# Performance work log

Measured on AMD Instinct MI355X. Metric: run time of the kernel, lower is better.

Reference implementation:

```python
import jax, jax.numpy as jnp
import numpy as np

EMB = 512
GP = 128
NH = 8
HD = EMB // NH  # 64
B = 2
S = 1024


def _rel_shift(x):
    # Faithful port of DoubleAttentionLayer._rel_shift (pads dim 1, reinterprets
    # (B, J+1, K, n) as (J+1, B, K, n), drops first slice). Row-major reshape
    # semantics match torch .view on contiguous tensors exactly.
    Bsz, J, K, N = x.shape
    zp = jnp.zeros((Bsz, 1, K, N), x.dtype)
    xp = jnp.concatenate([zp, x], axis=1).reshape(J + 1, Bsz, K, N)
    return xp[1:].reshape(Bsz, J, K, N)


def _layernorm(x):
    # nn.LayerNorm(emb_dim, elementwise_affine=False), eps=1e-5
    m = jnp.mean(x, axis=-1, keepdims=True)
    v = jnp.var(x, axis=-1, keepdims=True)
    return (x - m) / jnp.sqrt(v + 1e-5)


def _attention(q, k, v, Bc, Bp, gpe, mask, Wp_w, Wp_b):
    Bsz, J, E = q.shape
    K = k.shape[1]
    # content scores
    qc = jnp.tanh((q + Bc).reshape(Bsz, J, NH, HD))
    kh = jnp.tanh(k.reshape(Bsz, K, NH, HD))
    ctx = jnp.einsum('bjnd,bknd->bjkn', qc, kh)
    # position scores (tanh before reshape in source for qp -- elementwise, same math)
    qp = jnp.tanh(q + Bp).reshape(Bsz, J, NH, HD)
    kp = jnp.tanh((gpe @ Wp_w + Wp_b).reshape(Bsz, -1, NH, HD))
    pos = jnp.einsum('bjnd,bknd->bjkn', qp, kp)
    pad = ctx.shape[2] - pos.shape[2]  # static; 0 in this configuration
    if pad > 0:
        # replicate-pad pos at front of k dim; constant(0)-pad mask (torch F.pad defaults)
        pos = jnp.concatenate([jnp.broadcast_to(pos[:, :, :1], (Bsz, J, pad, NH)), pos], axis=2)
        mask = jnp.concatenate([jnp.zeros(mask.shape[:2] + (pad, mask.shape[3]), mask.dtype), mask], axis=2)
    pos = _rel_shift(pos)
    att = (ctx + pos) / (HD ** 0.5) - 1e30 * mask
    att = jax.nn.softmax(att, axis=2)
    vh = jnp.tanh(v.reshape(Bsz, K, NH, HD))
    return jnp.einsum('bjkn,bknd->bjnd', att, vh).reshape(Bsz, J, E)


def setup_inputs() -> dict:
    key = jax.random.key(0)
    ks = jax.random.split(key, 12)
    u_emb = jax.random.normal(ks[0], (B, S, EMB), jnp.float32)
    f_emb = jax.random.normal(ks[1], (B, S, EMB), jnp.float32)
    gpe = jax.random.normal(ks[2], (B, S, GP), jnp.float32)
    # causal masks: 1 where attention is disallowed, broadcast over heads
    causal = (1.0 - jnp.tril(jnp.ones((S, S), jnp.float32)))[None, :, :, None]
    u_mask = jnp.broadcast_to(causal, (B, S, S, 1))
    f_mask = jnp.broadcast_to(causal, (B, S, S, 1))
    w = 0.02
    Wq_w = w * jax.random.normal(ks[3], (EMB, EMB), jnp.float32)
    Wq_b = jnp.zeros((EMB,), jnp.float32)
    Wkv_w = w * jax.random.normal(ks[4], (EMB, 2 * EMB), jnp.float32)
    Wkv_b = jnp.zeros((2 * EMB,), jnp.float32)
    Wp_w = w * jax.random.normal(ks[5], (GP, EMB), jnp.float32)
    Wp_b = jnp.zeros((EMB,), jnp.float32)
    Wu_w = w * jax.random.normal(ks[6], (EMB, EMB), jnp.float32)
    Wu_b = jnp.zeros((EMB,), jnp.float32)
    Bfc = 0.2 * jax.random.normal(ks[7], (1, 1, EMB), jnp.float32)
    Bfp = 0.2 * jax.random.normal(ks[8], (1, 1, EMB), jnp.float32)
    Buc = 0.2 * jax.random.normal(ks[9], (1, 1, EMB), jnp.float32)
    Bup = 0.2 * jax.random.normal(ks[10], (1, 1, EMB), jnp.float32)
    return {"u_emb": u_emb, "f_emb": f_emb, "gpe": gpe, "u_mask": u_mask, "f_mask": f_mask,
            "Wq_w": Wq_w, "Wq_b": Wq_b, "Wkv_w": Wkv_w, "Wkv_b": Wkv_b,
            "Wp_w": Wp_w, "Wp_b": Wp_b, "Wu_w": Wu_w, "Wu_b": Wu_b,
            "Bfc": Bfc, "Bfp": Bfp, "Buc": Buc, "Bup": Bup}


def reference(u_emb, f_emb, gpe, u_mask, f_mask, Wq_w, Wq_b, Wkv_w, Wkv_b,
              Wp_w, Wp_b, Wu_w, Wu_b, Bfc, Bfp, Buc, Bup):
    # first_part=True path: f_mem = f_emb (memory buffer registration has no output effect)
    q_u = f_emb @ Wu_w + Wu_b
    kv = f_emb @ Wkv_w + Wkv_b
    k, v = jnp.split(kv, 2, axis=-1)
    u_out = _layernorm(u_emb + _attention(q_u, k, v, Buc, Bup, gpe, u_mask, Wp_w, Wp_b))
    # last_layer=False: second attention over f stream
    q_f = f_emb @ Wq_w + Wq_b
    f_out = _layernorm(f_emb + _attention(q_f, k, v, Bfc, Bfp, gpe, f_mask, Wp_w, Wp_b))
    return (u_out, f_out)
```

## Files before the change

### kernel.cpp

```cpp
#include <hip/hip_runtime.h>
#include <math.h>

#define EMB 512
#define NH 8
#define HD 64
#define BB 2
#define SS 1024
#define ROWS (BB * SS)

typedef __attribute__((ext_vector_type(8))) short bhalf8;
typedef __attribute__((ext_vector_type(4))) float f32x4;
typedef __attribute__((ext_vector_type(8))) unsigned short us8;
typedef unsigned short ushort_t;

__device__ __forceinline__ unsigned short f2bf(float x) {
  unsigned u = __float_as_uint(x);
  u = (u + 0x7FFFu + ((u >> 16) & 1u)) >> 16;
  return (unsigned short)u;
}
__device__ __forceinline__ float bf2f(unsigned short v) {
  return __uint_as_float(((unsigned)v) << 16);
}
__device__ __forceinline__ float fast_tanh(float x) {
  x = fminf(15.f, fmaxf(-15.f, x));
  const float e = __expf(2.f * x);
  return (e - 1.f) / (e + 1.f);
}

__global__ __launch_bounds__(256, 3) void projpe_kernel(
    const float* __restrict__ f_emb, const float* __restrict__ gpe,
    const float* __restrict__ Wu, const float* __restrict__ Wq,
    const float* __restrict__ Wkv, const float* __restrict__ Wp,
    const float* __restrict__ Wu_b, const float* __restrict__ Wq_b,
    const float* __restrict__ Wkv_b, const float* __restrict__ Wp_b,
    const float* __restrict__ Buc, const float* __restrict__ Bup,
    const float* __restrict__ Bfc, const float* __restrict__ Bfp,
    ushort_t* __restrict__ Qcomb, ushort_t* __restrict__ Kcomb,
    ushort_t* __restrict__ vhT) {
  const int bx = blockIdx.x;
  const int mb = blockIdx.y * 128;
  const int tid = threadIdx.x;
  const int w = tid >> 6, lane = tid & 63;
  const int ln = lane & 15, quad = lane >> 4;
  const int wm = (w >> 1) * 64, wn = (w & 1) * 32;

  __shared__ __align__(16) ushort_t sA[128 * 72];
  __shared__ __align__(16) ushort_t sB[64 * 72];

  if (bx == 0 && blockIdx.y == 0) {
    const int t2 = tid >> 7, rem = tid & 127;
    const int h = rem >> 4, d4 = (rem & 15) * 4;
    *(ushort4*)&Qcomb[((size_t)t2 * ROWS + 1023) * 1024 + h * 128 + 64 + d4] =
        make_ushort4(0, 0, 0, 0);
  }

  const bool isPe = (bx >= 32);
  const int nb = isPe ? 0 : bx * 64;
  const int npbase = isPe ? (bx - 32) * 64 : 0;
  const float* Af = isPe ? gpe : f_emb;
  const int lda = isPe ? 128 : 512;
  const int trips = isPe ? 2 : 8;

  const float* Wsrc;
  int Nw, coff;
  if (isPe) { Wsrc = Wp; Nw = 512; coff = npbase; }
  else if (nb < 512) { Wsrc = Wu; Nw = 512; coff = nb; }
  else if (nb < 1024) { Wsrc = Wq; Nw = 512; coff = nb - 512; }
  else { Wsrc = Wkv; Nw = 1024; coff = nb - 1024; }

  const int bn = tid & 63;
  const int bk0 = (tid >> 6) * 16;

  f32x4 acc[4][2];
#pragma unroll
  for (int rt = 0; rt < 4; ++rt)
#pragma unroll
    for (int ct = 0; ct < 2; ++ct) acc[rt][ct] = (f32x4){0.f, 0.f, 0.f, 0.f};

  float4 qa[8];
  float qbw[16];
#pragma unroll
  for (int i = 0; i < 4; ++i) {
    const int idx = tid + i * 256;
    const size_t base = (size_t)(mb + (idx >> 3)) * lda + (idx & 7) * 8;
    qa[2 * i] = *(const float4*)&Af[base];
    qa[2 * i + 1] = *(const float4*)&Af[base + 4];
  }
#pragma unroll
  for (int j = 0; j < 16; ++j)
    qbw[j] = Wsrc[(size_t)(bk0 + j) * Nw + coff + bn];

  for (int t0 = 0; t0 < trips; ++t0) {
    __syncthreads();
#pragma unroll
    for (int i = 0; i < 4; ++i) {
      const int idx = tid + i * 256;
      us8 o;
      const float4 a = qa[2 * i], b = qa[2 * i + 1];
      o[0] = f2bf(a.x); o[1] = f2bf(a.y); o[2] = f2bf(a.z); o[3] = f2bf(a.w);
      o[4] = f2bf(b.x); o[5] = f2bf(b.y); o[6] = f2bf(b.z); o[7] = f2bf(b.w);
      *(us8*)&sA[(idx >> 3) * 72 + (idx & 7) * 8] = o;
    }
    {
      us8 o0, o1;
#pragma unroll
      for (int j = 0; j < 8; ++j) {
        o0[j] = f2bf(qbw[j]);
        o1[j] = f2bf(qbw[8 + j]);
      }
      *(us8*)&sB[bn * 72 + bk0] = o0;
      *(us8*)&sB[bn * 72 + bk0 + 8] = o1;
    }
    __syncthreads();
    if (t0 < trips - 1) {
      const int k1 = (t0 + 1) * 64;
#pragma unroll
      for (int i = 0; i < 4; ++i) {
        const int idx = tid + i * 256;
        const size_t base = (size_t)(mb + (idx >> 3)) * lda + k1 + (idx & 7) * 8;
        qa[2 * i] = *(const float4*)&Af[base];
        qa[2 * i + 1] = *(const float4*)&Af[base + 4];
      }
#pragma unroll
      for (int j = 0; j < 16; ++j)
        qbw[j] = Wsrc[(size_t)(k1 + bk0 + j) * Nw + coff + bn];
    }
#pragma unroll
    for (int kc = 0; kc < 2; ++kc) {
      bhalf8 af[4], bf_[2];
#pragma unroll
      for (int rt = 0; rt < 4; ++rt)
        af[rt] =
            *(const bhalf8*)&sA[(wm + rt * 16 + ln) * 72 + kc * 32 + quad * 8];
#pragma unroll
      for (int ct = 0; ct < 2; ++ct)
        bf_[ct] =
            *(const bhalf8*)&sB[(wn + ct * 16 + ln) * 72 + kc * 32 + quad * 8];
#pragma unroll
      for (int rt = 0; rt < 4; ++rt)
#pragma unroll
        for (int ct = 0; ct < 2; ++ct)
          acc[rt][ct] = __builtin_amdgcn_mfma_f32_16x16x32_bf16(
              af[rt], bf_[ct], acc[rt][ct], 0, 0, 0);
    }
  }

  __syncthreads();
  ushort_t* sOut = sA;

  if (!isPe && nb >= 1536) {
#pragma unroll
    for (int ct = 0; ct < 2; ++ct) {
      const int nl = wn + ct * 16 + ln;
      const float wb = Wkv_b[nb + nl - 1024];
#pragma unroll
      for (int rt = 0; rt < 4; ++rt)
#pragma unroll
        for (int r = 0; r < 4; ++r) {
          const int ml = wm + rt * 16 + quad * 4 + r;
          sOut[nl * 136 + ml] = f2bf(fast_tanh(acc[rt][ct][r] + wb));
        }
    }
    __syncthreads();
    const int b = mb >> 10, mo = mb & 1023;
#pragma unroll
    for (int i = 0; i < 4; ++i) {
      const int idx = tid + i * 256;
      const int nl = idx >> 4, m8 = (idx & 15) * 8;
      const us8 v = *(const us8*)&sOut[nl * 136 + m8];
      *(us8*)&vhT[((size_t)b * 512 + (nb - 1536) + nl) * 1024 + mo + m8] = v;
    }
  } else {
    const float* WB =
        isPe ? Wp_b : (nb < 512 ? Wu_b : (nb < 1024 ? Wq_b : Wkv_b));
    const int woff =
        isPe ? npbase : (nb < 512 ? nb : (nb < 1024 ? nb - 512 : nb - 1024));
    const bool rawDump = (!isPe && nb < 1024);
#pragma unroll
    for (int ct = 0; ct < 2; ++ct) {
      const int nl = wn + ct * 16 + ln;
      const float wb = WB[woff + nl];
#pragma unroll
      for (int rt = 0; rt < 4; ++rt)
#pragma unroll
        for (int r = 0; r < 4; ++r) {
          const int ml = wm + rt * 16 + quad * 4 + r;
          const float v = acc[rt][ct][r] + wb;
          sOut[ml * 72 + nl] = f2bf(rawDump ? v : fast_tanh(v));
        }
    }
    __syncthreads();
#pragma unroll
    for (int i = 0; i < 4; ++i) {
      const int idx = tid + i * 256;
      const int rr = idx >> 3, c8 = (idx & 7) * 8;
      const int m = mb + rr;
      const us8 v = *(const us8*)&sOut[rr * 72 + c8];
      if (isPe) {
        const int n = npbase + c8;
        const int h = n >> 6;
        *(us8*)&Kcomb[(size_t)m * 1024 + h * 128 + 64 + (n & 63)] = v;
      } else if (nb < 1024) {
        const int strm = nb >= 512 ? 1 : 0;
        const int n = (nb - strm * 512) + c8;
        const int h = n >> 6;
        const float* BC = strm ? Bfc : Buc;
        const float* BP = strm ? Bfp : Bup;
        float bcA[8], bpA[8];
        *(float4*)&bcA[0] = *(const float4*)&BC[n];
        *(float4*)&bcA[4] = *(const float4*)&BC[n + 4];
        *(float4*)&bpA[0] = *(const float4*)&BP[n];
        *(float4*)&bpA[4] = *(const float4*)&BP[n + 4];
        us8 oc, op;
#pragma unroll
        for (int jj = 0; jj < 8; ++jj) {
          const float vv = bf2f((unsigned short)v[jj]);
          oc[jj] = f2bf(fast_tanh(vv + bcA[jj]));
          op[jj] = f2bf(fast_tanh(vv + bpA[jj]));
        }
        *(us8*)&Qcomb[((size_t)strm * ROWS + m) * 1024 + h * 128 + (n & 63)] =
            oc;
        if (m != 0) {
          const int mp = (m < 1024) ? m - 1 : m;
          *(us8*)&Qcomb[((size_t)strm * ROWS + mp) * 1024 + h * 128 + 64 +
                        (n & 63)] = op;
        }
      } else {
        const int n = (nb - 1024) + c8;
        const int h = n >> 6;
        *(us8*)&Kcomb[(size_t)m * 1024 + h * 128 + (n & 63)] = v;
      }
    }
  }
}

__global__ __launch_bounds__(256, 2) void attn_kernel(
    const ushort_t* __restrict__ Qcomb, const ushort_t* __restrict__ Kcomb,
    const ushort_t* __restrict__ vhT, ushort_t* __restrict__ attO) {
  const int bid = blockIdx.x;
  const int tid = threadIdx.x;
  const int w = tid >> 6, lane = tid & 63;
  const int ln = lane & 15, quad = lane >> 4;

  __shared__ __align__(16) ushort_t sQ[64 * 136];
  __shared__ __align__(16) ushort_t sK[64 * 136];
  __shared__ __align__(16) ushort_t sV[64 * 72];
  __shared__ __align__(16) ushort_t sP[64 * 72];

  const int jt = (bid < 256) ? (15 - (bid >> 5)) : ((bid - 256) >> 5);
  const int c = bid & 31, t = c >> 4, b = (c >> 3) & 1, h = c & 7;

  uint4 qq[4], pk[4], pv[2];
#pragma unroll
  for (int i = 0; i < 4; ++i) {
    const int idx = tid + i * 256;
    qq[i] = *(const uint4*)&Qcomb[((size_t)t * ROWS + b * SS + jt * 64 +
                                   (idx >> 4)) * 1024 + h * 128 +
                                  (idx & 15) * 8];
    pk[i] = *(const uint4*)&Kcomb[((size_t)b * SS + (idx >> 4)) * 1024 +
                                  h * 128 + (idx & 15) * 8];
  }
#pragma unroll
  for (int i = 0; i < 2; ++i) {
    const int idx = tid + i * 256;
    pv[i] = *(const uint4*)&vhT[((size_t)b * 512 + h * 64 + (idx >> 3)) * 1024 +
                                (idx & 7) * 8];
  }
#pragma unroll
  for (int i = 0; i < 4; ++i) {
    const int idx = tid + i * 256;
    *(uint4*)&sQ[(idx >> 4) * 136 + (idx & 15) * 8] = qq[i];
  }
  __syncthreads();

  bhalf8 aq[4];
#pragma unroll
  for (int kc = 0; kc < 4; ++kc)
    aq[kc] = *(const bhalf8*)&sQ[(w * 16 + ln) * 136 + kc * 32 + quad * 8];

  f32x4 oacc[4];
#pragma unroll
  for (int ct = 0; ct < 4; ++ct) oacc[ct] = (f32x4){0.f, 0.f, 0.f, 0.f};
  float lsum[4] = {0.f, 0.f, 0.f, 0.f};

  for (int kt = 0; kt <= jt; ++kt) {
    if (kt > 0) __syncthreads();
#pragma unroll
    for (int i = 0; i < 4; ++i) {
      const int idx = tid + i * 256;
      *(uint4*)&sK[(idx >> 4) * 136 + (idx & 15) * 8] = pk[i];
    }
#pragma unroll
    for (int i = 0; i < 2; ++i) {
      const int idx = tid + i * 256;
      *(uint4*)&sV[(idx >> 3) * 72 + (idx & 7) * 8] = pv[i];
    }
    __syncthreads();
    if (kt < jt) {
      const int k1 = (kt + 1) * 64;
#pragma unroll
      for (int i = 0; i < 4; ++i) {
        const int idx = tid + i * 256;
        pk[i] = *(const uint4*)&Kcomb[((size_t)b * SS + k1 + (idx >> 4)) *
                                          1024 + h * 128 + (idx & 15) * 8];
      }
#pragma unroll
      for (int i = 0; i < 2; ++i) {
        const int idx = tid + i * 256;
        pv[i] = *(const uint4*)&vhT[((size_t)b * 512 + h * 64 + (idx >> 3)) *
                                        1024 + k1 + (idx & 7) * 8];
      }
    }

    f32x4 sacc[4];
#pragma unroll
    for (int ct = 0; ct < 4; ++ct) {
      sacc[ct] = (f32x4){0.f, 0.f, 0.f, 0.f};
#pragma unroll
      for (int kc = 0; kc < 4; ++kc) {
        const bhalf8 bk =
            *(const bhalf8*)&sK[(ct * 16 + ln) * 136 + kc * 32 + quad * 8];
        sacc[ct] = __builtin_amdgcn_mfma_f32_16x16x32_bf16(aq[kc], bk,
                                                           sacc[ct], 0, 0, 0);
      }
    }

    const bool diag = (kt == jt);
#pragma unroll
    for (int ct = 0; ct < 4; ++ct)
#pragma unroll
      for (int r = 0; r < 4; ++r) {
        float p;
        if (diag && (ct * 16 + ln > w * 16 + quad * 4 + r))
          p = 0.f;
        else
          p = __expf(sacc[ct][r] * 0.125f - 16.f);
        sacc[ct][r] = p;
        lsum[r] += p;
      }

#pragma unroll
    for (int ct = 0; ct < 4; ++ct)
#pragma unroll
      for (int r = 0; r < 4; ++r)
        sP[(w * 16 + quad * 4 + r) * 72 + ct * 16 + ln] = f2bf(sacc[ct][r]);

#pragma unroll
    for (int kc = 0; kc < 2; ++kc) {
      const bhalf8 ap =
          *(const bhalf8*)&sP[(w * 16 + ln) * 72 + kc * 32 + quad * 8];
#pragma unroll
      for (int ct = 0; ct < 4; ++ct) {
        const bhalf8 bv =
            *(const bhalf8*)&sV[(ct * 16 + ln) * 72 + kc * 32 + quad * 8];
        oacc[ct] = __builtin_amdgcn_mfma_f32_16x16x32_bf16(ap, bv, oacc[ct],
                                                           0, 0, 0);
      }
    }
  }

#pragma unroll
  for (int r = 0; r < 4; ++r) {
    float s = lsum[r];
    s += __shfl_xor(s, 1);
    s += __shfl_xor(s, 2);
    s += __shfl_xor(s, 4);
    s += __shfl_xor(s, 8);
    const float inv = 1.f / s;
    const int j = jt * 64 + w * 16 + quad * 4 + r;
    const size_t orow = ((size_t)t * ROWS + b * SS + j) * 512 + h * 64;
#pragma unroll
    for (int ct = 0; ct < 4; ++ct)
      attO[orow + ct * 16 + ln] = f2bf(oacc[ct][r] * inv);
  }
}

__global__ __launch_bounds__(64) void ln_kernel(
    const float* __restrict__ u_emb, const float* __restrict__ f_emb,
    const ushort_t* __restrict__ attO, float* __restrict__ out) {
  const int rid = blockIdx.x;
  const int t = rid >> 11, row = rid & 2047;
  const float* resid = t ? f_emb : u_emb;
  const int tid = threadIdx.x;
  const size_t base = (size_t)row * 512;
  const size_t obase = ((size_t)t * ROWS + row) * 512;
  const int o = tid * 8;

  const us8 a = *(const us8*)&attO[obase + o];
  const float4 r0 = *(const float4*)&resid[base + o];
  const float4 r1 = *(const float4*)&resid[base + o + 4];
  float y[8];
  y[0] = r0.x + bf2f((unsigned short)a[0]);
  y[1] = r0.y + bf2f((unsigned short)a[1]);
  y[2] = r0.z + bf2f((unsigned short)a[2]);
  y[3] = r0.w + bf2f((unsigned short)a[3]);
  y[4] = r1.x + bf2f((unsigned short)a[4]);
  y[5] = r1.y + bf2f((unsigned short)a[5]);
  y[6] = r1.z + bf2f((unsigned short)a[6]);
  y[7] = r1.w + bf2f((unsigned short)a[7]);

  float s = 0.f, q = 0.f;
#pragma unroll
  for (int i = 0; i < 8; ++i) {
    s += y[i];
    q += y[i] * y[i];
  }
#pragma unroll
  for (int off = 1; off < 64; off <<= 1) {
    s += __shfl_xor(s, off);
    q += __shfl_xor(q, off);
  }
  const float mean = s * (1.f / 512.f);
  const float var = q * (1.f / 512.f) - mean * mean;
  const float rstd = rsqrtf(var + 1e-5f);

  float4 o0, o1;
  o0.x = (y[0] - mean) * rstd; o0.y = (y[1] - mean) * rstd;
  o0.z = (y[2] - mean) * rstd; o0.w = (y[3] - mean) * rstd;
  o1.x = (y[4] - mean) * rstd; o1.y = (y[5] - mean) * rstd;
  o1.z = (y[6] - mean) * rstd; o1.w = (y[7] - mean) * rstd;
  *(float4*)&out[obase + o] = o0;
  *(float4*)&out[obase + o + 4] = o1;
}

extern "C" void kernel_launch(void* const* d_in, const int* in_sizes, int n_in,
                              void* d_out, int out_size, void* d_ws,
                              size_t ws_size, hipStream_t stream) {
  (void)in_sizes; (void)n_in; (void)out_size; (void)ws_size;
  const float* u_emb = (const float*)d_in[0];
  const float* f_emb = (const float*)d_in[1];
  const float* gpe = (const float*)d_in[2];
  const float* Wq_w = (const float*)d_in[5];
  const float* Wq_b = (const float*)d_in[6];
  const float* Wkv_w = (const float*)d_in[7];
  const float* Wkv_b = (const float*)d_in[8];
  const float* Wp_w = (const float*)d_in[9];
  const float* Wp_b = (const float*)d_in[10];
  const float* Wu_w = (const float*)d_in[11];
  const float* Wu_b = (const float*)d_in[12];
  const float* Bfc = (const float*)d_in[13];
  const float* Bfp = (const float*)d_in[14];
  const float* Buc = (const float*)d_in[15];
  const float* Bup = (const float*)d_in[16];
  float* out = (float*)d_out;

  ushort_t* ws = (ushort_t*)d_ws;
  const size_t SZ = (size_t)ROWS * EMB;
  ushort_t* Qcomb = ws;
  ushort_t* Kcomb = ws + 4 * SZ;
  ushort_t* vhT = ws + 6 * SZ;
  ushort_t* attO = ws + 7 * SZ;

  dim3 blk(256);
  hipLaunchKernelGGL(projpe_kernel, dim3(40, 16), blk, 0, stream, f_emb, gpe,
                     Wu_w, Wq_w, Wkv_w, Wp_w, Wu_b, Wq_b, Wkv_b, Wp_b, Buc,
                     Bup, Bfc, Bfp, Qcomb, Kcomb, vhT);
  hipLaunchKernelGGL(attn_kernel, dim3(512), blk, 0, stream, Qcomb, Kcomb, vhT,
                     attO);
  hipLaunchKernelGGL(ln_kernel, dim3(4096), dim3(64), 0, stream, u_emb, f_emb,
                     attO, out);
}
```

Before: 170.8 us.

## Split long causal attention rows across two blocks and merge partials in layernorm

Query tiles in the upper half (jt 8-15) now have their key range split between two blocks. Each block writes an unnormalized partial output and a row sum, and the layernorm kernel adds the two partials and normalizes. Without a running max, the fixed exp offset makes the two partials combine exactly. The change also loads Q fragments straight from global memory instead of staging them in shared memory, raises occupancy to 3 blocks per SM, replaces the rounded bf16 conversion of P with truncation, and packs 4 rows per layernorm block. The aim is better load balance and more blocks in flight, at the cost of extra partial-buffer traffic and a small precision loss.

```diff
diff --git a/kernel.cpp b/kernel.cpp
--- a/kernel.cpp
+++ b/kernel.cpp
@@ -234,57 +234,70 @@
   }
 }
 
-__global__ __launch_bounds__(256, 2) void attn_kernel(
+__global__ __launch_bounds__(256, 3) void attn_kernel(
     const ushort_t* __restrict__ Qcomb, const ushort_t* __restrict__ Kcomb,
-    const ushort_t* __restrict__ vhT, ushort_t* __restrict__ attO) {
+    const ushort_t* __restrict__ vhT, ushort_t* __restrict__ attO,
+    ushort_t* __restrict__ Opart, float* __restrict__ lpart) {
   const int bid = blockIdx.x;
   const int tid = threadIdx.x;
   const int w = tid >> 6, lane = tid & 63;
   const int ln = lane & 15, quad = lane >> 4;
 
-  __shared__ __align__(16) ushort_t sQ[64 * 136];
   __shared__ __align__(16) ushort_t sK[64 * 136];
   __shared__ __align__(16) ushort_t sV[64 * 72];
   __shared__ __align__(16) ushort_t sP[64 * 72];
 
-  const int jt = (bid < 256) ? (15 - (bid >> 5)) : ((bid - 256) >> 5);
-  const int c = bid & 31, t = c >> 4, b = (c >> 3) & 1, h = c & 7;
-
-  uint4 qq[4], pk[4], pv[2];
+  int jt, kt0, kt1, half;
+  bool isHalf;
+  const int c = bid & 31;
+  if (bid < 512) {
+    isHalf = true;
+    const int uu = bid >> 5;
+    jt = 15 - (uu >> 1);
+    half = uu & 1;
+    const int h1 = (jt + 2) >> 1;
+    kt0 = half ? h1 : 0;
+    kt1 = half ? jt : (h1 - 1);
+  } else {
+    isHalf = false;
+    half = 0;
+    jt = 7 - ((bid - 512) >> 5);
+    kt0 = 0;
+    kt1 = jt;
+  }
+  const int t = c >> 4, b = (c >> 3) & 1, h = c & 7;
+
+  bhalf8 aq[4];
+  {
+    const size_t qbase =
+        ((size_t)t * ROWS + b * SS + jt * 64 + w * 16 + ln) * 1024 + h * 128 +
+        quad * 8;
+#pragma unroll
+    for (int kc = 0; kc < 4; ++kc)
+      aq[kc] = *(const bhalf8*)&Qcomb[qbase + kc * 32];
+  }
+
+  uint4 pk[4], pv[2];
 #pragma unroll
   for (int i = 0; i < 4; ++i) {
     const int idx = tid + i * 256;
-    qq[i] = *(const uint4*)&Qcomb[((size_t)t * ROWS + b * SS + jt * 64 +
-                                   (idx >> 4)) * 1024 + h * 128 +
-                                  (idx & 15) * 8];
-    pk[i] = *(const uint4*)&Kcomb[((size_t)b * SS + (idx >> 4)) * 1024 +
-                                  h * 128 + (idx & 15) * 8];
+    pk[i] = *(const uint4*)&Kcomb[((size_t)b * SS + kt0 * 64 + (idx >> 4)) *
+                                      1024 + h * 128 + (idx & 15) * 8];
   }
 #pragma unroll
   for (int i = 0; i < 2; ++i) {
     const int idx = tid + i * 256;
     pv[i] = *(const uint4*)&vhT[((size_t)b * 512 + h * 64 + (idx >> 3)) * 1024 +
-                                (idx & 7) * 8];
-  }
-#pragma unroll
-  for (int i = 0; i < 4; ++i) {
-    const int idx = tid + i * 256;
-    *(uint4*)&sQ[(idx >> 4) * 136 + (idx & 15) * 8] = qq[i];
-  }
-  __syncthreads();
-
-  bhalf8 aq[4];
-#pragma unroll
-  for (int kc = 0; kc < 4; ++kc)
-    aq[kc] = *(const bhalf8*)&sQ[(w * 16 + ln) * 136 + kc * 32 + quad * 8];
+                                kt0 * 64 + (idx & 7) * 8];
+  }
 
   f32x4 oacc[4];
 #pragma unroll
   for (int ct = 0; ct < 4; ++ct) oacc[ct] = (f32x4){0.f, 0.f, 0.f, 0.f};
   float lsum[4] = {0.f, 0.f, 0.f, 0.f};
 
-  for (int kt = 0; kt <= jt; ++kt) {
-    if (kt > 0) __syncthreads();
+  for (int kt = kt0; kt <= kt1; ++kt) {
+    if (kt > kt0) __syncthreads();
 #pragma unroll
     for (int i = 0; i < 4; ++i) {
       const int idx = tid + i * 256;
@@ -296,7 +309,7 @@
       *(uint4*)&sV[(idx >> 3) * 72 + (idx & 7) * 8] = pv[i];
     }
     __syncthreads();
-    if (kt < jt) {
+    if (kt < kt1) {
       const int k1 = (kt + 1) * 64;
 #pragma unroll
       for (int i = 0; i < 4; ++i) {
@@ -343,7 +356,8 @@
     for (int ct = 0; ct < 4; ++ct)
 #pragma unroll
       for (int r = 0; r < 4; ++r)
-        sP[(w * 16 + quad * 4 + r) * 72 + ct * 16 + ln] = f2bf(sacc[ct][r]);
+        sP[(w * 16 + quad * 4 + r) * 72 + ct * 16 + ln] =
+            (ushort_t)(__float_as_uint(sacc[ct][r]) >> 16);
 
 #pragma unroll
     for (int kc = 0; kc < 2; ++kc) {
@@ -366,38 +380,60 @@
     s += __shfl_xor(s, 2);
     s += __shfl_xor(s, 4);
     s += __shfl_xor(s, 8);
-    const float inv = 1.f / s;
     const int j = jt * 64 + w * 16 + quad * 4 + r;
-    const size_t orow = ((size_t)t * ROWS + b * SS + j) * 512 + h * 64;
-#pragma unroll
-    for (int ct = 0; ct < 4; ++ct)
-      attO[orow + ct * 16 + ln] = f2bf(oacc[ct][r] * inv);
-  }
-}
-
-__global__ __launch_bounds__(64) void ln_kernel(
+    if (!isHalf) {
+      const float inv = 1.f / s;
+      const size_t orow = ((size_t)t * ROWS + b * SS + j) * 512 + h * 64;
+#pragma unroll
+      for (int ct = 0; ct < 4; ++ct)
+        attO[orow + ct * 16 + ln] = f2bf(oacc[ct][r] * inv);
+    } else {
+      const int slot = half * 4 + t * 2 + b;
+      const size_t prow = ((size_t)slot * 512 + (j - 512)) * 512 + h * 64;
+#pragma unroll
+      for (int ct = 0; ct < 4; ++ct)
+        Opart[prow + ct * 16 + ln] = f2bf(oacc[ct][r]);
+      if (ln == 0)
+        lpart[((size_t)slot * 512 + (j - 512)) * 8 + h] = s;
+    }
+  }
+}
+
+__global__ __launch_bounds__(256) void ln_kernel(
     const float* __restrict__ u_emb, const float* __restrict__ f_emb,
-    const ushort_t* __restrict__ attO, float* __restrict__ out) {
-  const int rid = blockIdx.x;
+    const ushort_t* __restrict__ attO, const ushort_t* __restrict__ Opart,
+    const float* __restrict__ lpart, float* __restrict__ out) {
+  const int rid = blockIdx.x * 4 + (threadIdx.x >> 6);
+  const int lane = threadIdx.x & 63;
   const int t = rid >> 11, row = rid & 2047;
+  const int b = row >> 10, j = row & 1023;
   const float* resid = t ? f_emb : u_emb;
-  const int tid = threadIdx.x;
   const size_t base = (size_t)row * 512;
   const size_t obase = ((size_t)t * ROWS + row) * 512;
-  const int o = tid * 8;
-
-  const us8 a = *(const us8*)&attO[obase + o];
+  const int o = lane * 8;
+
   const float4 r0 = *(const float4*)&resid[base + o];
   const float4 r1 = *(const float4*)&resid[base + o + 4];
+  float ra[8] = {r0.x, r0.y, r0.z, r0.w, r1.x, r1.y, r1.z, r1.w};
   float y[8];
-  y[0] = r0.x + bf2f((unsigned short)a[0]);
-  y[1] = r0.y + bf2f((unsigned short)a[1]);
-  y[2] = r0.z + bf2f((unsigned short)a[2]);
-  y[3] = r0.w + bf2f((unsigned short)a[3]);
-  y[4] = r1.x + bf2f((unsigned short)a[4]);
-  y[5] = r1.y + bf2f((unsigned short)a[5]);
-  y[6] = r1.z + bf2f((unsigned short)a[6]);
-  y[7] = r1.w + bf2f((unsigned short)a[7]);
+  if (j < 512) {
+    const us8 a = *(const us8*)&attO[obase + o];
+#pragma unroll
+    for (int i = 0; i < 8; ++i) y[i] = ra[i] + bf2f((unsigned short)a[i]);
+  } else {
+    const int h = lane >> 3;
+    const int s0 = t * 2 + b, s1 = 4 + t * 2 + b;
+    const size_t pr = (size_t)(j - 512);
+    const float l = lpart[((size_t)s0 * 512 + pr) * 8 + h] +
+                    lpart[((size_t)s1 * 512 + pr) * 8 + h];
+    const float inv = 1.f / l;
+    const us8 a0 = *(const us8*)&Opart[((size_t)s0 * 512 + pr) * 512 + o];
+    const us8 a1 = *(const us8*)&Opart[((size_t)s1 * 512 + pr) * 512 + o];
+#pragma unroll
+    for (int i = 0; i < 8; ++i)
+      y[i] = ra[i] + (bf2f((unsigned short)a0[i]) +
+                      bf2f((unsigned short)a1[i])) * inv;
+  }
 
   float s = 0.f, q = 0.f;
 #pragma unroll
@@ -450,13 +486,15 @@
   ushort_t* Kcomb = ws + 4 * SZ;
   ushort_t* vhT = ws + 6 * SZ;
   ushort_t* attO = ws + 7 * SZ;
+  ushort_t* Opart = ws + 9 * SZ;
+  float* lpart = (float*)(ws + 11 * SZ);
 
   dim3 blk(256);
   hipLaunchKernelGGL(projpe_kernel, dim3(40, 16), blk, 0, stream, f_emb, gpe,
                      Wu_w, Wq_w, Wkv_w, Wp_w, Wu_b, Wq_b, Wkv_b, Wp_b, Buc,
                      Bup, Bfc, Bfp, Qcomb, Kcomb, vhT);
-  hipLaunchKernelGGL(attn_kernel, dim3(512), blk, 0, stream, Qcomb, Kcomb, vhT,
-                     attO);
-  hipLaunchKernelGGL(ln_kernel, dim3(4096), dim3(64), 0, stream, u_emb, f_emb,
-                     attO, out);
-}
+  hipLaunchKernelGGL(attn_kernel, dim3(768), blk, 0, stream, Qcomb, Kcomb, vhT,
+                     attO, Opart, lpart);
+  hipLaunchKernelGGL(ln_kernel, dim3(1024), blk, 0, stream, u_emb, f_emb, attO,
+                     Opart, lpart, out);
+}
```

After: 170.9 us. About the same (+0.1%).

## Balance causal attention with stream-K tile split, atomics, and async LDS loads

Applied to the files above, without the earlier changes.

Replaces the per-row-tile attention blocks with a stream-K style schedule. The 4352 causal (jt,kt) tiles are spread evenly over 512 blocks, 8 or 9 tiles each, and partial numerators and row sums are accumulated with fp32 atomics into buffers zeroed by the projection kernel. K and V are staged through double-buffered LDS via global_load_lds with an XOR swizzle, and Q is loaded straight into registers. The goal is to remove the load imbalance of the triangular workload and hide load latency. In exchange it adds atomic traffic, a larger fp32 workspace, a truncating bf16 conversion for P, and a final normalisation step in the layernorm kernel, which is also regrouped to four rows per 256-thread block.

```diff
diff --git a/kernel.cpp b/kernel.cpp
--- a/kernel.cpp
+++ b/kernel.cpp
@@ -13,6 +13,13 @@
 typedef __attribute__((ext_vector_type(8))) unsigned short us8;
 typedef unsigned short ushort_t;
 
+typedef const __attribute__((address_space(1))) void gas_void;
+typedef __attribute__((address_space(3))) void las_void;
+
+__device__ __forceinline__ void gl2lds16(const void* g, void* l) {
+  __builtin_amdgcn_global_load_lds((gas_void*)g, (las_void*)l, 16, 0, 0);
+}
+
 __device__ __forceinline__ unsigned short f2bf(float x) {
   unsigned u = __float_as_uint(x);
   u = (u + 0x7FFFu + ((u >> 16) & 1u)) >> 16;
@@ -27,7 +34,7 @@
   return (e - 1.f) / (e + 1.f);
 }
 
-__global__ __launch_bounds__(256, 3) void projpe_kernel(
+__global__ __launch_bounds__(256, 4) void projpe_kernel(
     const float* __restrict__ f_emb, const float* __restrict__ gpe,
     const float* __restrict__ Wu, const float* __restrict__ Wq,
     const float* __restrict__ Wkv, const float* __restrict__ Wp,
@@ -36,7 +43,8 @@
     const float* __restrict__ Buc, const float* __restrict__ Bup,
     const float* __restrict__ Bfc, const float* __restrict__ Bfp,
     ushort_t* __restrict__ Qcomb, ushort_t* __restrict__ Kcomb,
-    ushort_t* __restrict__ vhT) {
+    ushort_t* __restrict__ vhT, float* __restrict__ Onum,
+    float* __restrict__ lpart) {
   const int bx = blockIdx.x;
   const int mb = blockIdx.y * 128;
   const int tid = threadIdx.x;
@@ -47,7 +55,16 @@
   __shared__ __align__(16) ushort_t sA[128 * 72];
   __shared__ __align__(16) ushort_t sB[64 * 72];
 
-  if (bx == 0 && blockIdx.y == 0) {
+  const int fb = blockIdx.y * 40 + bx;
+  if (fb < 512) {
+    const float4 z4 = {0.f, 0.f, 0.f, 0.f};
+#pragma unroll
+    for (int i = 0; i < 4; ++i)
+      ((float4*)Onum)[(size_t)fb * 1024 + i * 256 + tid] = z4;
+  } else {
+    lpart[(fb - 512) * 256 + tid] = 0.f;
+  }
+  if (fb == 0) {
     const int t2 = tid >> 7, rem = tid & 127;
     const int h = rem >> 4, d4 = (rem & 15) * 4;
     *(ushort4*)&Qcomb[((size_t)t2 * ROWS + 1023) * 1024 + h * 128 + 64 + d4] =
@@ -236,80 +253,82 @@
 
 __global__ __launch_bounds__(256, 2) void attn_kernel(
     const ushort_t* __restrict__ Qcomb, const ushort_t* __restrict__ Kcomb,
-    const ushort_t* __restrict__ vhT, ushort_t* __restrict__ attO) {
+    const ushort_t* __restrict__ vhT, float* __restrict__ Onum,
+    float* __restrict__ lpart) {
   const int bid = blockIdx.x;
   const int tid = threadIdx.x;
   const int w = tid >> 6, lane = tid & 63;
   const int ln = lane & 15, quad = lane >> 4;
 
-  __shared__ __align__(16) ushort_t sQ[64 * 136];
-  __shared__ __align__(16) ushort_t sK[64 * 136];
-  __shared__ __align__(16) ushort_t sV[64 * 72];
+  __shared__ __align__(16) ushort_t sK[2 * 64 * 128];
+  __shared__ __align__(16) ushort_t sV[2 * 64 * 64];
   __shared__ __align__(16) ushort_t sP[64 * 72];
 
-  const int jt = (bid < 256) ? (15 - (bid >> 5)) : ((bid - 256) >> 5);
-  const int c = bid & 31, t = c >> 4, b = (c >> 3) & 1, h = c & 7;
-
-  uint4 qq[4], pk[4], pv[2];
-#pragma unroll
-  for (int i = 0; i < 4; ++i) {
-    const int idx = tid + i * 256;
-    qq[i] = *(const uint4*)&Qcomb[((size_t)t * ROWS + b * SS + jt * 64 +
-                                   (idx >> 4)) * 1024 + h * 128 +
-                                  (idx & 15) * 8];
-    pk[i] = *(const uint4*)&Kcomb[((size_t)b * SS + (idx >> 4)) * 1024 +
-                                  h * 128 + (idx & 15) * 8];
-  }
-#pragma unroll
-  for (int i = 0; i < 2; ++i) {
-    const int idx = tid + i * 256;
-    pv[i] = *(const uint4*)&vhT[((size_t)b * 512 + h * 64 + (idx >> 3)) * 1024 +
-                                (idx & 7) * 8];
-  }
-#pragma unroll
-  for (int i = 0; i < 4; ++i) {
-    const int idx = tid + i * 256;
-    *(uint4*)&sQ[(idx >> 4) * 136 + (idx & 15) * 8] = qq[i];
-  }
-  __syncthreads();
+  const int G0 = (bid * 17) >> 1;
+  const int G1 = ((bid + 1) * 17) >> 1;
+  const int cnt = G1 - G0;
+
+  int c = G0 / 136;
+  int u = G0 - c * 136;
+  int jt = (int)((sqrtf(8.f * u + 1.f) - 1.f) * 0.5f);
+  while ((jt + 1) * (jt + 2) / 2 <= u) ++jt;
+  while (jt * (jt + 1) / 2 > u) --jt;
+  int kt = u - jt * (jt + 1) / 2;
+  int t = c >> 4, b = (c >> 3) & 1, h = c & 7;
+
+  const int l4 = lane >> 4, p15 = lane & 15;
+  const int l3 = lane >> 3, l7 = lane & 7;
+#define STAGE_KV(B_, H_, KT_, BUF_)                                          \
+  {                                                                          \
+    const size_t kb_ = ((size_t)(B_)*SS + (KT_)*64) * 1024 + (H_)*128;       \
+    ushort_t* bk_ = sK + (BUF_)*8192;                                        \
+    _Pragma("unroll") for (int s_ = 0; s_ < 4; ++s_) {                       \
+      const int q_ = w * 4 + s_;                                             \
+      const int r_ = q_ * 4 + l4;                                            \
+      const int gl_ = p15 ^ (r_ & 7);                                        \
+      gl2lds16(&Kcomb[kb_ + (size_t)r_ * 1024 + gl_ * 8], &bk_[q_ * 512]);   \
+    }                                                                        \
+    const size_t vb_ = ((size_t)(B_)*512 + (H_)*64) * 1024 + (KT_)*64;       \
+    ushort_t* bv_ = sV + (BUF_)*4096;                                        \
+    _Pragma("unroll") for (int s_ = 0; s_ < 2; ++s_) {                       \
+      const int q_ = w * 2 + s_;                                             \
+      const int r_ = q_ * 8 + l3;                                            \
+      const int gl_ = l7 ^ (r_ & 7);                                         \
+      gl2lds16(&vhT[vb_ + (size_t)r_ * 1024 + gl_ * 8], &bv_[q_ * 512]);     \
+    }                                                                        \
+  }
 
   bhalf8 aq[4];
-#pragma unroll
-  for (int kc = 0; kc < 4; ++kc)
-    aq[kc] = *(const bhalf8*)&sQ[(w * 16 + ln) * 136 + kc * 32 + quad * 8];
+#define LOAD_AQ(T_, B_, H_, JT_)                                             \
+  {                                                                          \
+    const size_t qb_ =                                                       \
+        ((size_t)(T_)*ROWS + (B_)*SS + (JT_)*64 + w * 16 + ln) * 1024 +      \
+        (H_)*128 + quad * 8;                                                 \
+    _Pragma("unroll") for (int kc_ = 0; kc_ < 4; ++kc_) aq[kc_] =            \
+        *(const bhalf8*)&Qcomb[qb_ + kc_ * 32];                              \
+  }
+
+  STAGE_KV(b, h, kt, 0);
+  LOAD_AQ(t, b, h, jt);
 
   f32x4 oacc[4];
 #pragma unroll
   for (int ct = 0; ct < 4; ++ct) oacc[ct] = (f32x4){0.f, 0.f, 0.f, 0.f};
   float lsum[4] = {0.f, 0.f, 0.f, 0.f};
 
-  for (int kt = 0; kt <= jt; ++kt) {
-    if (kt > 0) __syncthreads();
-#pragma unroll
-    for (int i = 0; i < 4; ++i) {
-      const int idx = tid + i * 256;
-      *(uint4*)&sK[(idx >> 4) * 136 + (idx & 15) * 8] = pk[i];
-    }
-#pragma unroll
-    for (int i = 0; i < 2; ++i) {
-      const int idx = tid + i * 256;
-      *(uint4*)&sV[(idx >> 3) * 72 + (idx & 7) * 8] = pv[i];
-    }
+  for (int it = 0; it < cnt; ++it) {
     __syncthreads();
-    if (kt < jt) {
-      const int k1 = (kt + 1) * 64;
-#pragma unroll
-      for (int i = 0; i < 4; ++i) {
-        const int idx = tid + i * 256;
-        pk[i] = *(const uint4*)&Kcomb[((size_t)b * SS + k1 + (idx >> 4)) *
-                                          1024 + h * 128 + (idx & 15) * 8];
-      }
-#pragma unroll
-      for (int i = 0; i < 2; ++i) {
-        const int idx = tid + i * 256;
-        pv[i] = *(const uint4*)&vhT[((size_t)b * 512 + h * 64 + (idx >> 3)) *
-                                        1024 + k1 + (idx & 7) * 8];
-      }
+    const ushort_t* bK = sK + (it & 1) * 8192;
+    const ushort_t* bV = sV + (it & 1) * 4096;
+
+    int c2 = c, jt2 = jt, kt2 = kt + 1;
+    if (kt2 > jt) {
+      jt2 = jt + 1; kt2 = 0;
+      if (jt2 > 15) { c2 = c + 1; jt2 = 0; }
+    }
+    if (it < cnt - 1) {
+      const int b2 = (c2 >> 3) & 1, h2 = c2 & 7;
+      STAGE_KV(b2, h2, kt2, ((it + 1) & 1));
     }
 
     f32x4 sacc[4];
@@ -318,8 +337,8 @@
       sacc[ct] = (f32x4){0.f, 0.f, 0.f, 0.f};
 #pragma unroll
       for (int kc = 0; kc < 4; ++kc) {
-        const bhalf8 bk =
-            *(const bhalf8*)&sK[(ct * 16 + ln) * 136 + kc * 32 + quad * 8];
+        const bhalf8 bk = *(const bhalf8*)&bK[(ct * 16 + ln) * 128 +
+                                             (((kc * 4 + quad) ^ l7) << 3)];
         sacc[ct] = __builtin_amdgcn_mfma_f32_16x16x32_bf16(aq[kc], bk,
                                                            sacc[ct], 0, 0, 0);
       }
@@ -343,7 +362,8 @@
     for (int ct = 0; ct < 4; ++ct)
 #pragma unroll
       for (int r = 0; r < 4; ++r)
-        sP[(w * 16 + quad * 4 + r) * 72 + ct * 16 + ln] = f2bf(sacc[ct][r]);
+        sP[(w * 16 + quad * 4 + r) * 72 + ct * 16 + ln] =
+            (ushort_t)(__float_as_uint(sacc[ct][r]) >> 16);
 
 #pragma unroll
     for (int kc = 0; kc < 2; ++kc) {
@@ -351,53 +371,67 @@
           *(const bhalf8*)&sP[(w * 16 + ln) * 72 + kc * 32 + quad * 8];
 #pragma unroll
       for (int ct = 0; ct < 4; ++ct) {
-        const bhalf8 bv =
-            *(const bhalf8*)&sV[(ct * 16 + ln) * 72 + kc * 32 + quad * 8];
+        const bhalf8 bv = *(const bhalf8*)&bV[(ct * 16 + ln) * 64 +
+                                             (((kc * 4 + quad) ^ l7) << 3)];
         oacc[ct] = __builtin_amdgcn_mfma_f32_16x16x32_bf16(ap, bv, oacc[ct],
                                                            0, 0, 0);
       }
     }
-  }
-
-#pragma unroll
-  for (int r = 0; r < 4; ++r) {
-    float s = lsum[r];
-    s += __shfl_xor(s, 1);
-    s += __shfl_xor(s, 2);
-    s += __shfl_xor(s, 4);
-    s += __shfl_xor(s, 8);
-    const float inv = 1.f / s;
-    const int j = jt * 64 + w * 16 + quad * 4 + r;
-    const size_t orow = ((size_t)t * ROWS + b * SS + j) * 512 + h * 64;
-#pragma unroll
-    for (int ct = 0; ct < 4; ++ct)
-      attO[orow + ct * 16 + ln] = f2bf(oacc[ct][r] * inv);
-  }
-}
-
-__global__ __launch_bounds__(64) void ln_kernel(
+
+    const bool rowEnd = (it == cnt - 1) || (jt2 != jt) || (c2 != c);
+    if (rowEnd) {
+#pragma unroll
+      for (int r = 0; r < 4; ++r) {
+        float s = lsum[r];
+        s += __shfl_xor(s, 1);
+        s += __shfl_xor(s, 2);
+        s += __shfl_xor(s, 4);
+        s += __shfl_xor(s, 8);
+        const int j = jt * 64 + w * 16 + quad * 4 + r;
+        if (ln == 0)
+          atomicAdd(&lpart[((((t * 2 + b) << 10) + j) << 3) + h], s);
+        const size_t orow = (((size_t)t * ROWS + b * SS + j) << 9) + h * 64;
+#pragma unroll
+        for (int ct = 0; ct < 4; ++ct)
+          atomicAdd(&Onum[orow + ct * 16 + ln], oacc[ct][r]);
+        lsum[r] = 0.f;
+      }
+#pragma unroll
+      for (int ct = 0; ct < 4; ++ct) oacc[ct] = (f32x4){0.f, 0.f, 0.f, 0.f};
+      if (it < cnt - 1) {
+        const int t2 = c2 >> 4, b2 = (c2 >> 3) & 1, h2 = c2 & 7;
+        LOAD_AQ(t2, b2, h2, jt2);
+      }
+    }
+    c = c2; jt = jt2; kt = kt2;
+    t = c >> 4; b = (c >> 3) & 1; h = c & 7;
+  }
+}
+
+__global__ __launch_bounds__(256) void ln_kernel(
     const float* __restrict__ u_emb, const float* __restrict__ f_emb,
-    const ushort_t* __restrict__ attO, float* __restrict__ out) {
-  const int rid = blockIdx.x;
+    const float* __restrict__ Onum, const float* __restrict__ lpart,
+    float* __restrict__ out) {
+  const int rid = blockIdx.x * 4 + (threadIdx.x >> 6);
+  const int lane = threadIdx.x & 63;
   const int t = rid >> 11, row = rid & 2047;
+  const int b = row >> 10, j = row & 1023;
   const float* resid = t ? f_emb : u_emb;
-  const int tid = threadIdx.x;
   const size_t base = (size_t)row * 512;
   const size_t obase = ((size_t)t * ROWS + row) * 512;
-  const int o = tid * 8;
-
-  const us8 a = *(const us8*)&attO[obase + o];
+  const int o = lane * 8;
+  const int h = lane >> 3;
+  const float inv = 1.f / lpart[((((t * 2 + b) << 10) + j) << 3) + h];
+
+  const float4 n0 = *(const float4*)&Onum[obase + o];
+  const float4 n1 = *(const float4*)&Onum[obase + o + 4];
   const float4 r0 = *(const float4*)&resid[base + o];
   const float4 r1 = *(const float4*)&resid[base + o + 4];
   float y[8];
-  y[0] = r0.x + bf2f((unsigned short)a[0]);
-  y[1] = r0.y + bf2f((unsigned short)a[1]);
-  y[2] = r0.z + bf2f((unsigned short)a[2]);
-  y[3] = r0.w + bf2f((unsigned short)a[3]);
-  y[4] = r1.x + bf2f((unsigned short)a[4]);
-  y[5] = r1.y + bf2f((unsigned short)a[5]);
-  y[6] = r1.z + bf2f((unsigned short)a[6]);
-  y[7] = r1.w + bf2f((unsigned short)a[7]);
+  y[0] = r0.x + n0.x * inv; y[1] = r0.y + n0.y * inv;
+  y[2] = r0.z + n0.z * inv; y[3] = r0.w + n0.w * inv;
+  y[4] = r1.x + n1.x * inv; y[5] = r1.y + n1.y * inv;
+  y[6] = r1.z + n1.z * inv; y[7] = r1.w + n1.w * inv;
 
   float s = 0.f, q = 0.f;
 #pragma unroll
@@ -449,14 +483,15 @@
   ushort_t* Qcomb = ws;
   ushort_t* Kcomb = ws + 4 * SZ;
   ushort_t* vhT = ws + 6 * SZ;
-  ushort_t* attO = ws + 7 * SZ;
+  float* Onum = (float*)(ws + 7 * SZ);
+  float* lpart = (float*)(ws + 11 * SZ);
 
   dim3 blk(256);
   hipLaunchKernelGGL(projpe_kernel, dim3(40, 16), blk, 0, stream, f_emb, gpe,
                      Wu_w, Wq_w, Wkv_w, Wp_w, Wu_b, Wq_b, Wkv_b, Wp_b, Buc,
-                     Bup, Bfc, Bfp, Qcomb, Kcomb, vhT);
+                     Bup, Bfc, Bfp, Qcomb, Kcomb, vhT, Onum, lpart);
   hipLaunchKernelGGL(attn_kernel, dim3(512), blk, 0, stream, Qcomb, Kcomb, vhT,
-                     attO);
-  hipLaunchKernelGGL(ln_kernel, dim3(4096), dim3(64), 0, stream, u_emb, f_emb,
-                     attO, out);
-}
+                     Onum, lpart);
+  hipLaunchKernelGGL(ln_kernel, dim3(1024), blk, 0, stream, u_emb, f_emb, Onum,
+                     lpart, out);
+}
```

Result: faster. 158.2 us (-7.4%).
